# Kernel optimization log

Hardware: AMD Instinct MI355X
Metric: run time of the kernel (lower is better)

## Reference

```python
import jax, jax.numpy as jnp
import numpy as np

B, D_IN, D_PROJ, N_CLS = 4096, 4096, 1024, 32
N_CHILD = (32, 64)


def setup_inputs() -> dict:
    key = jax.random.key(0)
    ks = jax.random.split(key, 12)
    std = 2e-05
    inp = {
        "x": jax.random.normal(ks[0], (B, D_IN), dtype=jnp.float32),
        "y": jax.random.randint(ks[1], (B,), 0, N_CLS, dtype=jnp.int32),
        # parent projection: Linear(D_IN, D_PROJ)
        "Wp": jax.random.normal(ks[2], (D_IN, D_PROJ), dtype=jnp.float32) * std,
        "bp": jnp.zeros((D_PROJ,), jnp.float32),
        # subclass projection: Linear(D_IN, D_PROJ)
        "Ws": jax.random.normal(ks[3], (D_IN, D_PROJ), dtype=jnp.float32) * std,
        "bs": jnp.zeros((D_PROJ,), jnp.float32),
        # parent classifier: Linear(D_PROJ, N_CLS)
        "Wc": jax.random.normal(ks[4], (D_PROJ, N_CLS), dtype=jnp.float32) * std,
        "bc": jnp.zeros((N_CLS,), jnp.float32),
        # child expert banks: level i has N_CLS experts of Linear(D_PROJ, N_CHILD[i])
        "cw0": jax.random.normal(ks[5], (N_CLS, N_CHILD[0], D_PROJ), dtype=jnp.float32) * std,
        "cb0": jnp.zeros((N_CLS, N_CHILD[0]), jnp.float32),
        "cw1": jax.random.normal(ks[6], (N_CLS, N_CHILD[1], D_PROJ), dtype=jnp.float32) * std,
        "cb1": jnp.zeros((N_CLS, N_CHILD[1]), jnp.float32),
    }
    return inp


def reference(x, y, Wp, bp, Ws, bs, Wc, bc, cw0, cb0, cw1, cb1):
    # dropout p = 0.0 -> identity
    parent_proj_embed = x @ Wp + bp                 # [B, D_PROJ]
    parent_logits = parent_proj_embed @ Wc + bc     # [B, N_CLS]
    child_proj_embed = x @ Ws + bs                  # [B, D_PROJ]
    # per-sample expert routing: gather the expert for label y[b], then batched matvec
    child_logits0 = jnp.einsum("bd,bnd->bn", child_proj_embed, cw0[y]) + cb0[y]  # [B, 32]
    child_logits1 = jnp.einsum("bd,bnd->bn", child_proj_embed, cw1[y]) + cb1[y]  # [B, 64]
    return (parent_logits, child_logits0, child_logits1, parent_proj_embed, child_proj_embed)
```

## Files before the change

### kernel.cpp

```cpp
#include <hip/hip_runtime.h>
#include <hip/hip_bf16.h>
#include <stdint.h>


typedef __attribute__((ext_vector_type(4))) float  floatx4;
typedef __attribute__((ext_vector_type(8))) short  shortx8;
typedef __attribute__((ext_vector_type(4))) short  shortx4;
typedef __attribute__((ext_vector_type(8))) __bf16 bf16x8;

static __device__ __forceinline__ ushort f32_to_bf16_rne(float f) {
  uint32_t u = __builtin_bit_cast(uint32_t, f);
  u += 0x7FFFu + ((u >> 16) & 1u);
  return (ushort)(u >> 16);
}
static __device__ __forceinline__ float bf16u_to_f32(ushort h) {
  uint32_t u = ((uint32_t)h) << 16;
  return __builtin_bit_cast(float, u);
}

static __device__ __forceinline__ void async_copy16(const void* g, void* lds) {
  __builtin_amdgcn_global_load_lds(
      (__attribute__((address_space(1))) void*)(uintptr_t)g,
      (__attribute__((address_space(3))) void*)(uintptr_t)lds,
      16, 0, 0);
}

#define BM 128
#define BN 128
#define BK 64

static __device__ __forceinline__ void gemm_core_128(
    const ushort* __restrict__ A, const ushort* __restrict__ B,
    int lda, int ldb, int K, int mTile, int nTile,
    ushort* lA, ushort* lB, floatx4 acc[4][4])
{
  const int t    = threadIdx.x;
  const int w    = t >> 6;
  const int lane = t & 63;
  const int wr   = w >> 1;
  const int wc   = w & 1;
  const int r16  = lane & 15;
  const int quad = lane >> 4;
  const int sr   = lane >> 3;
  const int sc   = lane & 7;

  const ushort* Abase = A + (size_t)(mTile * BM) * lda;
  const ushort* Bbase = B + (size_t)(nTile * BN) * ldb;

  for (int k0 = 0; k0 < K; k0 += BK) {
    #pragma unroll
    for (int c2 = 0; c2 < 4; ++c2) {
      const int r  = 32 * w + 8 * c2 + sr;
      const int gc = sc ^ (r & 7);
      async_copy16(Abase + (size_t)r * lda + k0 + gc * 8, lA + (32 * w + 8 * c2) * BK);
      async_copy16(Bbase + (size_t)r * ldb + k0 + gc * 8, lB + (32 * w + 8 * c2) * BK);
    }
    __syncthreads();

    #pragma unroll
    for (int ks = 0; ks < 2; ++ks) {
      bf16x8 af[4], bfv[4];
      const int pc = (((ks * 4) + quad) ^ (r16 & 7)) * 8;
      #pragma unroll
      for (int mi = 0; mi < 4; ++mi) {
        const int row = wr * 64 + mi * 16 + r16;
        af[mi] = *reinterpret_cast<const bf16x8*>(lA + row * BK + pc);
      }
      #pragma unroll
      for (int ni = 0; ni < 4; ++ni) {
        const int row = wc * 64 + ni * 16 + r16;
        bfv[ni] = *reinterpret_cast<const bf16x8*>(lB + row * BK + pc);
      }
      #pragma unroll
      for (int mi = 0; mi < 4; ++mi)
        #pragma unroll
        for (int ni = 0; ni < 4; ++ni)
          acc[mi][ni] = __builtin_amdgcn_mfma_f32_16x16x32_bf16(
              af[mi], bfv[ni], acc[mi][ni], 0, 0, 0);
    }
    __syncthreads();
  }
}


__global__ __launch_bounds__(256) void k_cast_x(const float* __restrict__ x,
                                                ushort* __restrict__ xb)
{
  const size_t i = ((size_t)blockIdx.x * 256 + threadIdx.x) * 8;
  floatx4 a = *reinterpret_cast<const floatx4*>(x + i);
  floatx4 b = *reinterpret_cast<const floatx4*>(x + i + 4);
  shortx8 o;
  o[0] = (short)f32_to_bf16_rne(a[0]); o[1] = (short)f32_to_bf16_rne(a[1]);
  o[2] = (short)f32_to_bf16_rne(a[2]); o[3] = (short)f32_to_bf16_rne(a[3]);
  o[4] = (short)f32_to_bf16_rne(b[0]); o[5] = (short)f32_to_bf16_rne(b[1]);
  o[6] = (short)f32_to_bf16_rne(b[2]); o[7] = (short)f32_to_bf16_rne(b[3]);
  *reinterpret_cast<shortx8*>(xb + i) = o;
}

__global__ __launch_bounds__(256) void k_transpose_w(const float* __restrict__ Wp,
                                                     const float* __restrict__ Ws,
                                                     ushort* __restrict__ Bt1)
{
  __shared__ __align__(16) ushort tile[64][72];
  const float* W = blockIdx.z ? Ws : Wp;
  const int kt = blockIdx.x;
  const int nt = blockIdx.y;
  const int t  = threadIdx.x;
  const int r  = t >> 4;
  const int c  = (t & 15) * 4;
  #pragma unroll
  for (int i = 0; i < 4; ++i) {
    const int kk = r + i * 16;
    floatx4 v = *reinterpret_cast<const floatx4*>(
        W + (size_t)(kt * 64 + kk) * 1024 + nt * 64 + c);
    tile[c + 0][kk] = f32_to_bf16_rne(v[0]);
    tile[c + 1][kk] = f32_to_bf16_rne(v[1]);
    tile[c + 2][kk] = f32_to_bf16_rne(v[2]);
    tile[c + 3][kk] = f32_to_bf16_rne(v[3]);
  }
  __syncthreads();
  const int nl = t >> 3;
  const int ch = t & 7;
  #pragma unroll
  for (int i = 0; i < 2; ++i) {
    const int n = nl + i * 32;
    shortx8 v = *reinterpret_cast<const shortx8*>(&tile[n][ch * 8]);
    *reinterpret_cast<shortx8*>(
        Bt1 + (size_t)(blockIdx.z * 1024 + nt * 64 + n) * 4096 + kt * 64 + ch * 8) = v;
  }
}

__global__ __launch_bounds__(256) void k_prep_bt2(const float* __restrict__ cw0,
                                                  const float* __restrict__ cw1,
                                                  const float* __restrict__ Wc,
                                                  ushort* __restrict__ Bt2)
{
  const int idx = (blockIdx.x * 256 + threadIdx.x) * 4;
  const int row = idx >> 10;
  const int k   = idx & 1023;
  float v0, v1, v2, v3;
  if (row < 1024) {
    floatx4 f = *reinterpret_cast<const floatx4*>(cw0 + idx);
    v0 = f[0]; v1 = f[1]; v2 = f[2]; v3 = f[3];
  } else if (row < 3072) {
    floatx4 f = *reinterpret_cast<const floatx4*>(cw1 + (size_t)(row - 1024) * 1024 + k);
    v0 = f[0]; v1 = f[1]; v2 = f[2]; v3 = f[3];
  } else if (row < 3104) {
    const int n = row - 3072;
    v0 = Wc[(k + 0) * 32 + n]; v1 = Wc[(k + 1) * 32 + n];
    v2 = Wc[(k + 2) * 32 + n]; v3 = Wc[(k + 3) * 32 + n];
  } else {
    v0 = v1 = v2 = v3 = 0.f;
  }
  shortx4 o;
  o[0] = (short)f32_to_bf16_rne(v0); o[1] = (short)f32_to_bf16_rne(v1);
  o[2] = (short)f32_to_bf16_rne(v2); o[3] = (short)f32_to_bf16_rne(v3);
  *reinterpret_cast<shortx4*>(Bt2 + idx) = o;
}


__global__ __launch_bounds__(256) void k_gemm1(
    const ushort* __restrict__ xb, const ushort* __restrict__ Bt1,
    const float* __restrict__ bp, const float* __restrict__ bs,
    float* __restrict__ outP, float* __restrict__ outS,
    ushort* __restrict__ Pb, ushort* __restrict__ Sb)
{
  __shared__ __align__(16) ushort lA[BM * BK];
  __shared__ __align__(16) ushort lB[BN * BK];
  floatx4 acc[4][4];
  const floatx4 z = {0.f, 0.f, 0.f, 0.f};
  #pragma unroll
  for (int i = 0; i < 4; ++i)
    #pragma unroll
    for (int j = 0; j < 4; ++j) acc[i][j] = z;

  gemm_core_128(xb, Bt1, 4096, 4096, 4096, blockIdx.x, blockIdx.y, lA, lB, acc);

  const int t = threadIdx.x, w = t >> 6, lane = t & 63;
  const int wr = w >> 1, wc = w & 1, r16 = lane & 15, quad = lane >> 4;
  const int sel = (blockIdx.y >= 8);
  const float* bias = sel ? bs : bp;
  float*  outF = sel ? outS : outP;
  ushort* outB = sel ? Sb : Pb;
  const int colbase = blockIdx.y * 128 - sel * 1024;
  #pragma unroll
  for (int mi = 0; mi < 4; ++mi) {
    #pragma unroll
    for (int ni = 0; ni < 4; ++ni) {
      const int n = colbase + wc * 64 + ni * 16 + r16;
      const float bv = bias[n];
      #pragma unroll
      for (int rg = 0; rg < 4; ++rg) {
        const int m = blockIdx.x * 128 + wr * 64 + mi * 16 + quad * 4 + rg;
        const float v = acc[mi][ni][rg] + bv;
        const size_t off = (size_t)m * 1024 + n;
        outF[off] = v;
        outB[off] = f32_to_bf16_rne(v);
      }
    }
  }
}

__global__ __launch_bounds__(256) void k_gemm2(
    const ushort* __restrict__ Sb, const ushort* __restrict__ Pb,
    const ushort* __restrict__ Bt2, const float* __restrict__ bc,
    ushort* __restrict__ dense2, float* __restrict__ outParent)
{
  __shared__ __align__(16) ushort lA[BM * BK];
  __shared__ __align__(16) ushort lB[BN * BK];
  floatx4 acc[4][4];
  const floatx4 z = {0.f, 0.f, 0.f, 0.f};
  #pragma unroll
  for (int i = 0; i < 4; ++i)
    #pragma unroll
    for (int j = 0; j < 4; ++j) acc[i][j] = z;

  const ushort* Ap = (blockIdx.y < 24) ? Sb : Pb;
  gemm_core_128(Ap, Bt2, 1024, 1024, 1024, blockIdx.x, blockIdx.y, lA, lB, acc);

  const int t = threadIdx.x, w = t >> 6, lane = t & 63;
  const int wr = w >> 1, wc = w & 1, r16 = lane & 15, quad = lane >> 4;
  if (blockIdx.y < 24) {
    const int nbase = blockIdx.y * 128;
    #pragma unroll
    for (int mi = 0; mi < 4; ++mi) {
      #pragma unroll
      for (int ni = 0; ni < 4; ++ni) {
        const int n = nbase + wc * 64 + ni * 16 + r16;
        #pragma unroll
        for (int rg = 0; rg < 4; ++rg) {
          const int m = blockIdx.x * 128 + wr * 64 + mi * 16 + quad * 4 + rg;
          dense2[(size_t)m * 3072 + n] = f32_to_bf16_rne(acc[mi][ni][rg]);
        }
      }
    }
  } else if (wc == 0) {
    #pragma unroll
    for (int mi = 0; mi < 4; ++mi) {
      #pragma unroll
      for (int ni = 0; ni < 2; ++ni) {
        const int nl = ni * 16 + r16;
        const float bv = bc[nl];
        #pragma unroll
        for (int rg = 0; rg < 4; ++rg) {
          const int m = blockIdx.x * 128 + wr * 64 + mi * 16 + quad * 4 + rg;
          outParent[(size_t)m * 32 + nl] = acc[mi][ni][rg] + bv;
        }
      }
    }
  }
}

__global__ __launch_bounds__(128) void k_gather(
    const int* __restrict__ y, const ushort* __restrict__ dense2,
    const float* __restrict__ cb0, const float* __restrict__ cb1,
    float* __restrict__ out0, float* __restrict__ out1)
{
  const int b = blockIdx.x;
  const int t = threadIdx.x;
  const int e = y[b];
  if (t < 32) {
    out0[b * 32 + t] =
        bf16u_to_f32(dense2[(size_t)b * 3072 + e * 32 + t]) + cb0[e * 32 + t];
  } else if (t < 96) {
    const int n = t - 32;
    out1[b * 64 + n] =
        bf16u_to_f32(dense2[(size_t)b * 3072 + 1024 + e * 64 + n]) + cb1[e * 64 + n];
  }
}


extern "C" void kernel_launch(void* const* d_in, const int* in_sizes, int n_in,
                              void* d_out, int out_size, void* d_ws, size_t ws_size,
                              hipStream_t stream) {
  const float* x   = (const float*)d_in[0];
  const int*   y   = (const int*)  d_in[1];
  const float* Wp  = (const float*)d_in[2];
  const float* bp  = (const float*)d_in[3];
  const float* Ws  = (const float*)d_in[4];
  const float* bs  = (const float*)d_in[5];
  const float* Wc  = (const float*)d_in[6];
  const float* bc  = (const float*)d_in[7];
  const float* cw0 = (const float*)d_in[8];
  const float* cb0 = (const float*)d_in[9];
  const float* cw1 = (const float*)d_in[10];
  const float* cb1 = (const float*)d_in[11];

  float* out = (float*)d_out;
  float* parent_logits = out;
  float* child0        = out + 131072;
  float* child1        = out + 262144;
  float* P             = out + 524288;
  float* S             = out + 4718592;

  char* ws = (char*)d_ws;
  ushort* xb     = (ushort*)(ws);
  ushort* dense2 = (ushort*)(ws);
  ushort* Bt1    = (ushort*)(ws + 33554432);
  ushort* Pb     = (ushort*)(ws + 50331648);
  ushort* Sb     = (ushort*)(ws + 58720256);
  ushort* Bt2    = (ushort*)(ws + 67108864);

  k_cast_x     <<<8192, 256, 0, stream>>>(x, xb);
  k_transpose_w<<<dim3(64, 16, 2), 256, 0, stream>>>(Wp, Ws, Bt1);
  k_prep_bt2   <<<3200, 256, 0, stream>>>(cw0, cw1, Wc, Bt2);
  k_gemm1      <<<dim3(32, 16), 256, 0, stream>>>(xb, Bt1, bp, bs, P, S, Pb, Sb);
  k_gemm2      <<<dim3(32, 25), 256, 0, stream>>>(Sb, Pb, Bt2, bc, dense2, parent_logits);
  k_gather     <<<4096, 128, 0, stream>>>(y, dense2, cb0, cb1, child0, child1);
}
```

Measured before the change: 303.0 us.

## Route child experts by bucketing samples per label instead of dense all-expert GEMM

Replaces the dense child GEMM over all 32 experts plus a gather with a per-label bucketed grouped GEMM. A small bucketing kernel builds a sample permutation and per-class offsets, and the head kernel gathers rows of the projected embedding for each class and multiplies only by that class's expert weights. The aim is to cut roughly 32x redundant expert FLOPs and drop the large intermediate buffer and the gather kernel. In exchange it adds a single-block bucketing kernel, gathered row loads, and padded 128-row expert tiles (96 rows used), and many of the launched blocks exit early.

```diff
diff --git a/kernel.cpp b/kernel.cpp
--- a/kernel.cpp
+++ b/kernel.cpp
@@ -12,10 +12,6 @@
   uint32_t u = __builtin_bit_cast(uint32_t, f);
   u += 0x7FFFu + ((u >> 16) & 1u);
   return (ushort)(u >> 16);
-}
-static __device__ __forceinline__ float bf16u_to_f32(ushort h) {
-  uint32_t u = ((uint32_t)h) << 16;
-  return __builtin_bit_cast(float, u);
 }
 
 static __device__ __forceinline__ void async_copy16(const void* g, void* lds) {
@@ -28,6 +24,33 @@
 #define BM 128
 #define BN 128
 #define BK 64
+
+static __device__ __forceinline__ void mfma_bk_step(
+    const ushort* lA, const ushort* lB, floatx4 acc[4][4],
+    int wr, int wc, int r16, int quad)
+{
+  #pragma unroll
+  for (int ks = 0; ks < 2; ++ks) {
+    bf16x8 af[4], bfv[4];
+    const int pc = (((ks * 4) + quad) ^ (r16 & 7)) * 8;
+    #pragma unroll
+    for (int mi = 0; mi < 4; ++mi) {
+      const int row = wr * 64 + mi * 16 + r16;
+      af[mi] = *reinterpret_cast<const bf16x8*>(lA + row * BK + pc);
+    }
+    #pragma unroll
+    for (int ni = 0; ni < 4; ++ni) {
+      const int row = wc * 64 + ni * 16 + r16;
+      bfv[ni] = *reinterpret_cast<const bf16x8*>(lB + row * BK + pc);
+    }
+    #pragma unroll
+    for (int mi = 0; mi < 4; ++mi)
+      #pragma unroll
+      for (int ni = 0; ni < 4; ++ni)
+        acc[mi][ni] = __builtin_amdgcn_mfma_f32_16x16x32_bf16(
+            af[mi], bfv[ni], acc[mi][ni], 0, 0, 0);
+  }
+}
 
 static __device__ __forceinline__ void gemm_core_128(
     const ushort* __restrict__ A, const ushort* __restrict__ B,
@@ -51,33 +74,12 @@
     #pragma unroll
     for (int c2 = 0; c2 < 4; ++c2) {
       const int r  = 32 * w + 8 * c2 + sr;
-      const int gc = sc ^ (r & 7);
+      const int gc = sc ^ sr;
       async_copy16(Abase + (size_t)r * lda + k0 + gc * 8, lA + (32 * w + 8 * c2) * BK);
       async_copy16(Bbase + (size_t)r * ldb + k0 + gc * 8, lB + (32 * w + 8 * c2) * BK);
     }
     __syncthreads();
-
-    #pragma unroll
-    for (int ks = 0; ks < 2; ++ks) {
-      bf16x8 af[4], bfv[4];
-      const int pc = (((ks * 4) + quad) ^ (r16 & 7)) * 8;
-      #pragma unroll
-      for (int mi = 0; mi < 4; ++mi) {
-        const int row = wr * 64 + mi * 16 + r16;
-        af[mi] = *reinterpret_cast<const bf16x8*>(lA + row * BK + pc);
-      }
-      #pragma unroll
-      for (int ni = 0; ni < 4; ++ni) {
-        const int row = wc * 64 + ni * 16 + r16;
-        bfv[ni] = *reinterpret_cast<const bf16x8*>(lB + row * BK + pc);
-      }
-      #pragma unroll
-      for (int mi = 0; mi < 4; ++mi)
-        #pragma unroll
-        for (int ni = 0; ni < 4; ++ni)
-          acc[mi][ni] = __builtin_amdgcn_mfma_f32_16x16x32_bf16(
-              af[mi], bfv[ni], acc[mi][ni], 0, 0, 0);
-    }
+    mfma_bk_step(lA, lB, acc, wr, wc, r16, quad);
     __syncthreads();
   }
 }
@@ -130,32 +132,67 @@
   }
 }
 
-__global__ __launch_bounds__(256) void k_prep_bt2(const float* __restrict__ cw0,
-                                                  const float* __restrict__ cw1,
-                                                  const float* __restrict__ Wc,
-                                                  ushort* __restrict__ Bt2)
-{
-  const int idx = (blockIdx.x * 256 + threadIdx.x) * 4;
-  const int row = idx >> 10;
-  const int k   = idx & 1023;
-  float v0, v1, v2, v3;
-  if (row < 1024) {
-    floatx4 f = *reinterpret_cast<const floatx4*>(cw0 + idx);
-    v0 = f[0]; v1 = f[1]; v2 = f[2]; v3 = f[3];
-  } else if (row < 3072) {
-    floatx4 f = *reinterpret_cast<const floatx4*>(cw1 + (size_t)(row - 1024) * 1024 + k);
-    v0 = f[0]; v1 = f[1]; v2 = f[2]; v3 = f[3];
-  } else if (row < 3104) {
-    const int n = row - 3072;
-    v0 = Wc[(k + 0) * 32 + n]; v1 = Wc[(k + 1) * 32 + n];
-    v2 = Wc[(k + 2) * 32 + n]; v3 = Wc[(k + 3) * 32 + n];
+__global__ __launch_bounds__(256) void k_prep_w2(const float* __restrict__ cw0,
+                                                 const float* __restrict__ cw1,
+                                                 const float* __restrict__ Wc,
+                                                 ushort* __restrict__ cwb,
+                                                 ushort* __restrict__ Wcb)
+{
+  const int row = blockIdx.x;
+  const int k   = threadIdx.x * 4;
+  float v0 = 0.f, v1 = 0.f, v2 = 0.f, v3 = 0.f;
+  ushort* dst;
+  if (row < 4096) {
+    const int c = row >> 7, n = row & 127;
+    if (n < 32) {
+      floatx4 f = *reinterpret_cast<const floatx4*>(cw0 + (size_t)(c * 32 + n) * 1024 + k);
+      v0 = f[0]; v1 = f[1]; v2 = f[2]; v3 = f[3];
+    } else if (n < 96) {
+      floatx4 f = *reinterpret_cast<const floatx4*>(cw1 + (size_t)(c * 64 + (n - 32)) * 1024 + k);
+      v0 = f[0]; v1 = f[1]; v2 = f[2]; v3 = f[3];
+    }
+    dst = cwb + (size_t)row * 1024 + k;
   } else {
-    v0 = v1 = v2 = v3 = 0.f;
+    const int n = row - 4096;
+    if (n < 32) {
+      v0 = Wc[(k + 0) * 32 + n]; v1 = Wc[(k + 1) * 32 + n];
+      v2 = Wc[(k + 2) * 32 + n]; v3 = Wc[(k + 3) * 32 + n];
+    }
+    dst = Wcb + (size_t)n * 1024 + k;
   }
   shortx4 o;
   o[0] = (short)f32_to_bf16_rne(v0); o[1] = (short)f32_to_bf16_rne(v1);
   o[2] = (short)f32_to_bf16_rne(v2); o[3] = (short)f32_to_bf16_rne(v3);
-  *reinterpret_cast<shortx4*>(Bt2 + idx) = o;
+  *reinterpret_cast<shortx4*>(dst) = o;
+}
+
+__global__ __launch_bounds__(1024) void k_bucket(const int* __restrict__ y,
+                                                 int* __restrict__ perm,
+                                                 int* __restrict__ off)
+{
+  __shared__ int hist[32], base[32], cur[32];
+  const int t = threadIdx.x;
+  if (t < 32) { hist[t] = 0; cur[t] = 0; }
+  __syncthreads();
+  int yv[4];
+  #pragma unroll
+  for (int i = 0; i < 4; ++i) {
+    yv[i] = y[t * 4 + i];
+    atomicAdd(&hist[yv[i]], 1);
+  }
+  __syncthreads();
+  if (t == 0) {
+    int s = 0;
+    for (int c = 0; c < 32; ++c) { base[c] = s; off[c] = s; s += hist[c]; }
+    off[32] = s;
+  }
+  __syncthreads();
+  #pragma unroll
+  for (int i = 0; i < 4; ++i) {
+    const int c = yv[i];
+    const int p = atomicAdd(&cur[c], 1);
+    perm[base[c] + p] = t * 4 + i;
+  }
 }
 
 
@@ -201,10 +238,14 @@
   }
 }
 
-__global__ __launch_bounds__(256) void k_gemm2(
+__global__ __launch_bounds__(256) void k_head(
     const ushort* __restrict__ Sb, const ushort* __restrict__ Pb,
-    const ushort* __restrict__ Bt2, const float* __restrict__ bc,
-    ushort* __restrict__ dense2, float* __restrict__ outParent)
+    const ushort* __restrict__ cwb, const ushort* __restrict__ Wcb,
+    const int* __restrict__ perm, const int* __restrict__ off,
+    const float* __restrict__ cb0, const float* __restrict__ cb1,
+    const float* __restrict__ bc,
+    float* __restrict__ out0, float* __restrict__ out1,
+    float* __restrict__ outParent)
 {
   __shared__ __align__(16) ushort lA[BM * BK];
   __shared__ __align__(16) ushort lB[BN * BK];
@@ -215,57 +256,75 @@
     #pragma unroll
     for (int j = 0; j < 4; ++j) acc[i][j] = z;
 
-  const ushort* Ap = (blockIdx.y < 24) ? Sb : Pb;
-  gemm_core_128(Ap, Bt2, 1024, 1024, 1024, blockIdx.x, blockIdx.y, lA, lB, acc);
-
   const int t = threadIdx.x, w = t >> 6, lane = t & 63;
   const int wr = w >> 1, wc = w & 1, r16 = lane & 15, quad = lane >> 4;
-  if (blockIdx.y < 24) {
-    const int nbase = blockIdx.y * 128;
-    #pragma unroll
-    for (int mi = 0; mi < 4; ++mi) {
+
+  if (blockIdx.y == 32) {
+    gemm_core_128(Pb, Wcb, 1024, 1024, 1024, blockIdx.x, 0, lA, lB, acc);
+    if (wc == 0) {
+      #pragma unroll
+      for (int mi = 0; mi < 4; ++mi)
+        #pragma unroll
+        for (int ni = 0; ni < 2; ++ni) {
+          const int n = ni * 16 + r16;
+          const float bv = bc[n];
+          #pragma unroll
+          for (int rg = 0; rg < 4; ++rg) {
+            const int m = blockIdx.x * 128 + wr * 64 + mi * 16 + quad * 4 + rg;
+            outParent[(size_t)m * 32 + n] = acc[mi][ni][rg] + bv;
+          }
+        }
+    }
+    return;
+  }
+
+  const int c    = blockIdx.y;
+  const int off0 = off[c];
+  const int cnt  = off[c + 1] - off0;
+  const int m0   = blockIdx.x * BM;
+  if (m0 >= cnt) return;
+
+  const int sr = lane >> 3;
+  const int sc = lane & 7;
+  int rowSamp[4];
+  #pragma unroll
+  for (int c2 = 0; c2 < 4; ++c2) {
+    const int r = 32 * w + 8 * c2 + sr;
+    rowSamp[c2] = perm[off0 + min(m0 + r, cnt - 1)];
+  }
+  const ushort* Bbase = cwb + (size_t)c * 128 * 1024;
+
+  for (int k0 = 0; k0 < 1024; k0 += BK) {
+    #pragma unroll
+    for (int c2 = 0; c2 < 4; ++c2) {
+      const int r  = 32 * w + 8 * c2 + sr;
+      const int gc = sc ^ sr;
+      async_copy16(Sb + (size_t)rowSamp[c2] * 1024 + k0 + gc * 8,
+                   lA + (32 * w + 8 * c2) * BK);
+      async_copy16(Bbase + (size_t)r * 1024 + k0 + gc * 8,
+                   lB + (32 * w + 8 * c2) * BK);
+    }
+    __syncthreads();
+    mfma_bk_step(lA, lB, acc, wr, wc, r16, quad);
+    __syncthreads();
+  }
+
+  #pragma unroll
+  for (int mi = 0; mi < 4; ++mi) {
+    #pragma unroll
+    for (int rg = 0; rg < 4; ++rg) {
+      const int gm = m0 + wr * 64 + mi * 16 + quad * 4 + rg;
+      if (gm >= cnt) continue;
+      const int sample = perm[off0 + gm];
       #pragma unroll
       for (int ni = 0; ni < 4; ++ni) {
-        const int n = nbase + wc * 64 + ni * 16 + r16;
-        #pragma unroll
-        for (int rg = 0; rg < 4; ++rg) {
-          const int m = blockIdx.x * 128 + wr * 64 + mi * 16 + quad * 4 + rg;
-          dense2[(size_t)m * 3072 + n] = f32_to_bf16_rne(acc[mi][ni][rg]);
-        }
+        const int n = wc * 64 + ni * 16 + r16;
+        if (n < 32)
+          out0[(size_t)sample * 32 + n] = acc[mi][ni][rg] + cb0[c * 32 + n];
+        else if (n < 96)
+          out1[(size_t)sample * 64 + (n - 32)] = acc[mi][ni][rg] + cb1[c * 64 + (n - 32)];
       }
     }
-  } else if (wc == 0) {
-    #pragma unroll
-    for (int mi = 0; mi < 4; ++mi) {
-      #pragma unroll
-      for (int ni = 0; ni < 2; ++ni) {
-        const int nl = ni * 16 + r16;
-        const float bv = bc[nl];
-        #pragma unroll
-        for (int rg = 0; rg < 4; ++rg) {
-          const int m = blockIdx.x * 128 + wr * 64 + mi * 16 + quad * 4 + rg;
-          outParent[(size_t)m * 32 + nl] = acc[mi][ni][rg] + bv;
-        }
-      }
-    }
-  }
-}
-
-__global__ __launch_bounds__(128) void k_gather(
-    const int* __restrict__ y, const ushort* __restrict__ dense2,
-    const float* __restrict__ cb0, const float* __restrict__ cb1,
-    float* __restrict__ out0, float* __restrict__ out1)
-{
-  const int b = blockIdx.x;
-  const int t = threadIdx.x;
-  const int e = y[b];
-  if (t < 32) {
-    out0[b * 32 + t] =
-        bf16u_to_f32(dense2[(size_t)b * 3072 + e * 32 + t]) + cb0[e * 32 + t];
-  } else if (t < 96) {
-    const int n = t - 32;
-    out1[b * 64 + n] =
-        bf16u_to_f32(dense2[(size_t)b * 3072 + 1024 + e * 64 + n]) + cb1[e * 64 + n];
   }
 }
 
@@ -294,17 +353,21 @@
   float* S             = out + 4718592;
 
   char* ws = (char*)d_ws;
-  ushort* xb     = (ushort*)(ws);
-  ushort* dense2 = (ushort*)(ws);
-  ushort* Bt1    = (ushort*)(ws + 33554432);
-  ushort* Pb     = (ushort*)(ws + 50331648);
-  ushort* Sb     = (ushort*)(ws + 58720256);
-  ushort* Bt2    = (ushort*)(ws + 67108864);
+  ushort* xb   = (ushort*)(ws);
+  ushort* Bt1  = (ushort*)(ws + 33554432);
+  ushort* Pb   = (ushort*)(ws + 50331648);
+  ushort* Sb   = (ushort*)(ws + 58720256);
+  ushort* cwb  = (ushort*)(ws + 67108864);
+  ushort* Wcb  = (ushort*)(ws + 75497472);
+  int*    perm = (int*)   (ws + 75759616);
+  int*    offs = (int*)   (ws + 75776000);
 
   k_cast_x     <<<8192, 256, 0, stream>>>(x, xb);
   k_transpose_w<<<dim3(64, 16, 2), 256, 0, stream>>>(Wp, Ws, Bt1);
-  k_prep_bt2   <<<3200, 256, 0, stream>>>(cw0, cw1, Wc, Bt2);
+  k_prep_w2    <<<4224, 256, 0, stream>>>(cw0, cw1, Wc, cwb, Wcb);
+  k_bucket     <<<1, 1024, 0, stream>>>(y, perm, offs);
   k_gemm1      <<<dim3(32, 16), 256, 0, stream>>>(xb, Bt1, bp, bs, P, S, Pb, Sb);
-  k_gemm2      <<<dim3(32, 25), 256, 0, stream>>>(Sb, Pb, Bt2, bc, dense2, parent_logits);
-  k_gather     <<<4096, 128, 0, stream>>>(y, dense2, cb0, cb1, child0, child1);
-}
+  k_head       <<<dim3(32, 33), 256, 0, stream>>>(Sb, Pb, cwb, Wcb, perm, offs,
+                                                  cb0, cb1, bc,
+                                                  child0, child1, parent_logits);
+}
```

After: 324.0 us. 1.07x slower.
